# Kernel optimization log

Measured on AMD Instinct MI355X. Metric: run time of the kernel, lower is better.

## Reference

```python
import jax, jax.numpy as jnp
import numpy as np

B, L = 8, 12288
MASK_P = 0.01  # sparsity of the label-correlation adjacency


def setup_inputs() -> dict:
    key = jax.random.key(0)
    k1, k2, k3, k4 = jax.random.split(key, 4)
    predicts = jax.random.normal(k1, (B, L), dtype=jnp.float32)
    similarities = jax.random.uniform(k2, (B, B), dtype=jnp.float32)
    adj = jax.random.uniform(k3, (L, L), dtype=jnp.float32)
    adj_mask = jax.random.bernoulli(k4, MASK_P, (L, L))  # bool: lj in adjList[li]
    return {"predicts": predicts, "similarities": similarities,
            "adj": adj, "adj_mask": adj_mask}


def reference(predicts, similarities, adj, adj_mask):
    dt = predicts.dtype
    m = adj_mask.astype(dt)                      # [L, L]
    diag_m = jnp.diagonal(m)                     # [L]
    eye = jnp.eye(adj.shape[0], dtype=dt)
    # effective matrix: masked adjacency weight, else identity on diagonal
    b_eff = m * adj + eye * (1.0 - diag_m)[None, :]
    # relation_num per target label lj
    counts = jnp.sum(m, axis=0) + (1.0 - diag_m)  # [L]
    candidates = (predicts @ b_eff) / counts[None, :]          # [B, L]
    diff = predicts - similarities @ candidates                # [B, L]
    norms = jnp.sqrt(jnp.sum(diff * diff, axis=1))             # [B]
    valid = jnp.sum(similarities, axis=1) != 0                 # [B]
    cnt = jnp.sum(valid.astype(dt))
    total = jnp.sum(jnp.where(valid, norms, jnp.zeros((), dt)))
    return jnp.where(cnt == 0, jnp.zeros((), dt), total / jnp.maximum(cnt, 1.0))
```

## Files before the change

### kernel.cpp

```cpp
#include <hip/hip_runtime.h>
#include <hip/hip_bf16.h>
#include <stdint.h>

#define BB 8
#define LL 12288
#define NCB 12
#define NCH 96
#define RPC (LL / NCH)

#define WS_FLAGS 0
#define WS_SACC  16
#define WS_CNT   (WS_SACC + BB * LL)
#define WS_NORM2 (WS_CNT + LL)
#define WS_TOTAL (WS_NORM2 + 8)

__device__ __forceinline__ float bf2f(uint16_t u) {
  union { uint32_t i; float f; } v; v.i = ((uint32_t)u) << 16; return v.f;
}

__global__ void detect_kernel(const uint8_t* __restrict__ mask,
                              const uint8_t* __restrict__ adj,
                              int* __restrict__ flags) {
  __shared__ int s[6];
  int tid = threadIdx.x;
  if (tid < 6) s[tid] = 0;
  __syncthreads();
  int c[4] = {0, 0, 0, 0};
  int big = 0, hi = 0;
  const int N = 65536;
  for (int idx = tid; idx < N; idx += blockDim.x) {
    uint8_t v = mask[idx];
    if (v) { c[idx & 3]++; if (v >= 2) big++; }
    uint8_t a = adj[idx];
    if ((idx & 3) == 1 && a >= 0x80) hi++;
  }
  atomicAdd(&s[0], c[0]); atomicAdd(&s[1], c[1]);
  atomicAdd(&s[2], c[2]); atomicAdd(&s[3], c[3]);
  atomicAdd(&s[4], big);  atomicAdd(&s[5], hi);
  __syncthreads();
  if (tid == 0) {
    int width;
    int nzoff = s[1] + s[2] + s[3];
    if (nzoff == 0)             width = 4;
    else if (s[0] + s[1] == 0)  width = 4;
    else if (s[4] == 0)         width = 1;
    else                        width = 2;
    flags[0] = width;
    flags[1] = (s[5] == 0) ? 1 : 0;
  }
}

template <int MW, int FB>
__device__ void s1loop(const uint8_t* __restrict__ mask,
                       const uint8_t* __restrict__ adj,
                       float* __restrict__ sacc, float* __restrict__ cntw,
                       const float* __restrict__ sp,
                       int j0, int i0) {
  float acc[BB][4];
  float c4[4] = {0.f, 0.f, 0.f, 0.f};
#pragma unroll
  for (int b = 0; b < BB; b++)
    acc[b][0] = acc[b][1] = acc[b][2] = acc[b][3] = 0.f;

#pragma unroll 2
  for (int il = 0; il < RPC; ++il) {
    size_t e = (size_t)(i0 + il) * LL + j0;
    float a[4];
    if (FB) {
      ushort4 u = *reinterpret_cast<const ushort4*>(adj + e * 2);
      a[0] = bf2f(u.x); a[1] = bf2f(u.y); a[2] = bf2f(u.z); a[3] = bf2f(u.w);
    } else {
      float4 f = *reinterpret_cast<const float4*>(adj + e * 4);
      a[0] = f.x; a[1] = f.y; a[2] = f.z; a[3] = f.w;
    }
    int m[4];
    if (MW == 1) {
      uchar4 u = *reinterpret_cast<const uchar4*>(mask + e);
      m[0] = u.x != 0; m[1] = u.y != 0; m[2] = u.z != 0; m[3] = u.w != 0;
    } else if (MW == 2) {
      ushort4 u = *reinterpret_cast<const ushort4*>(mask + e * 2);
      m[0] = u.x != 0; m[1] = u.y != 0; m[2] = u.z != 0; m[3] = u.w != 0;
    } else {
      uint4 u = *reinterpret_cast<const uint4*>(mask + e * 4);
      m[0] = u.x != 0; m[1] = u.y != 0; m[2] = u.z != 0; m[3] = u.w != 0;
    }
#pragma unroll
    for (int k = 0; k < 4; k++) {
      a[k] = m[k] ? a[k] : 0.f;
      c4[k] += m[k] ? 1.f : 0.f;
    }
    float4 p0 = *reinterpret_cast<const float4*>(sp + il * BB);
    float4 p1 = *reinterpret_cast<const float4*>(sp + il * BB + 4);
    float pv[BB] = {p0.x, p0.y, p0.z, p0.w, p1.x, p1.y, p1.z, p1.w};
#pragma unroll
    for (int b = 0; b < BB; b++)
#pragma unroll
      for (int k = 0; k < 4; k++) acc[b][k] = fmaf(pv[b], a[k], acc[b][k]);
  }
#pragma unroll
  for (int b = 0; b < BB; b++)
#pragma unroll
    for (int k = 0; k < 4; k++)
      unsafeAtomicAdd(&sacc[b * LL + j0 + k], acc[b][k]);
#pragma unroll
  for (int k = 0; k < 4; k++) unsafeAtomicAdd(&cntw[j0 + k], c4[k]);
}

__global__ __launch_bounds__(256) void stage1(const uint8_t* __restrict__ mask,
                                              const uint8_t* __restrict__ adj,
                                              const uint8_t* __restrict__ pred,
                                              float* __restrict__ ws) {
  __shared__ float sp[RPC * BB];
  const int* fl = (const int*)ws;
  int mw = fl[0], fb = fl[1];
  int cb = blockIdx.x % NCB;
  int ch = blockIdx.x / NCB;
  int j0 = cb * 1024 + threadIdx.x * 4;
  int i0 = ch * RPC;
  for (int idx = threadIdx.x; idx < RPC * BB; idx += 256) {
    int b = idx / RPC, il = idx % RPC;
    float p = fb ? bf2f(reinterpret_cast<const uint16_t*>(pred)[b * LL + i0 + il])
                 : reinterpret_cast<const float*>(pred)[b * LL + i0 + il];
    sp[il * BB + b] = p;
  }
  __syncthreads();
  float* sacc = ws + WS_SACC;
  float* cntw = ws + WS_CNT;
  if (fb) {
    if (mw == 1)      s1loop<1, 1>(mask, adj, sacc, cntw, sp, j0, i0);
    else if (mw == 2) s1loop<2, 1>(mask, adj, sacc, cntw, sp, j0, i0);
    else              s1loop<4, 1>(mask, adj, sacc, cntw, sp, j0, i0);
  } else {
    if (mw == 1)      s1loop<1, 0>(mask, adj, sacc, cntw, sp, j0, i0);
    else if (mw == 2) s1loop<2, 0>(mask, adj, sacc, cntw, sp, j0, i0);
    else              s1loop<4, 0>(mask, adj, sacc, cntw, sp, j0, i0);
  }
}

__global__ __launch_bounds__(256) void stage23(const uint8_t* __restrict__ mask,
                                               const uint8_t* __restrict__ pred,
                                               const uint8_t* __restrict__ sim,
                                               float* __restrict__ ws) {
  const int* fl = (const int*)ws;
  int mw = fl[0], fb = fl[1];
  float* sacc = ws + WS_SACC;
  float* cntw = ws + WS_CNT;
  float* norm2 = ws + WS_NORM2;
  __shared__ float ssim[64];
  if (threadIdx.x < 64) {
    ssim[threadIdx.x] = fb ? bf2f(((const uint16_t*)sim)[threadIdx.x])
                           : ((const float*)sim)[threadIdx.x];
  }
  __syncthreads();
  int j = blockIdx.x * 256 + threadIdx.x;
  size_t ed = (size_t)j * LL + j;
  int mjj;
  if (mw == 1)      mjj = mask[ed] != 0;
  else if (mw == 2) mjj = ((const uint16_t*)mask)[ed] != 0;
  else              mjj = ((const uint32_t*)mask)[ed] != 0;
  float add = mjj ? 0.f : 1.f;
  float c = cntw[j] + add;
  float pj[BB], cv[BB];
#pragma unroll
  for (int b = 0; b < BB; b++)
    pj[b] = fb ? bf2f(((const uint16_t*)pred)[b * LL + j])
               : ((const float*)pred)[b * LL + j];
#pragma unroll
  for (int k = 0; k < BB; k++) cv[k] = (sacc[k * LL + j] + pj[k] * add) / c;
#pragma unroll
  for (int b = 0; b < BB; b++) {
    float t = pj[b];
#pragma unroll
    for (int k = 0; k < BB; k++) t = fmaf(-ssim[b * 8 + k], cv[k], t);
    float v = t * t;
#pragma unroll
    for (int off = 32; off > 0; off >>= 1) v += __shfl_down(v, off, 64);
    if ((threadIdx.x & 63) == 0) unsafeAtomicAdd(&norm2[b], v);
  }
}

__global__ void stage4(const uint8_t* __restrict__ sim,
                       uint8_t* __restrict__ out, float* __restrict__ ws) {
  if (threadIdx.x != 0) return;
  const int* fl = (const int*)ws;
  int fb = fl[1];
  float* norm2 = ws + WS_NORM2;
  float total = 0.f, cntv = 0.f;
  for (int b = 0; b < BB; b++) {
    float rs = 0.f;
    for (int k = 0; k < 8; k++)
      rs += fb ? bf2f(((const uint16_t*)sim)[b * 8 + k])
               : ((const float*)sim)[b * 8 + k];
    if (rs != 0.f) { cntv += 1.f; total += sqrtf(norm2[b]); }
  }
  float res = (cntv == 0.f) ? 0.f : total / fmaxf(cntv, 1.f);
  if (fb) *reinterpret_cast<__hip_bfloat16*>(out) = __float2bfloat16(res);
  else    *reinterpret_cast<float*>(out) = res;
}

extern "C" void kernel_launch(void* const* d_in, const int* in_sizes, int n_in,
                              void* d_out, int out_size, void* d_ws,
                              size_t ws_size, hipStream_t stream) {
  const uint8_t* pred = (const uint8_t*)d_in[0];
  const uint8_t* sim  = (const uint8_t*)d_in[1];
  const uint8_t* adj  = (const uint8_t*)d_in[2];
  const uint8_t* mask = (const uint8_t*)d_in[3];
  float* ws = (float*)d_ws;

  hipMemsetAsync(d_ws, 0, WS_TOTAL * sizeof(float), stream);
  detect_kernel<<<1, 256, 0, stream>>>(mask, adj, (int*)d_ws);
  stage1<<<NCB * NCH, 256, 0, stream>>>(mask, adj, pred, ws);
  stage23<<<LL / 256, 256, 0, stream>>>(mask, pred, sim, ws);
  stage4<<<1, 64, 0, stream>>>(sim, (uint8_t*)d_out, ws);
}
```

Baseline: 1.452 ms.

## Replace stage1 atomics with per-chunk partial buffers and separate reduction kernel

Each stage1 thread now handles 8 columns with wider vector loads, and the grid changes to 6 column blocks by 128 row chunks. The per-thread results are no longer accumulated with global float atomics. Each row chunk writes its own partial sums and counts to a workspace buffer, and a new reduce kernel sums the 128 partials. This removes atomic contention and the large memset, at the cost of an extra kernel launch and extra partial-buffer traffic. That traffic is about 50MB, which is small next to the 600MB+ adjacency read.

```diff
diff --git a/kernel.cpp b/kernel.cpp
--- a/kernel.cpp
+++ b/kernel.cpp
@@ -4,18 +4,31 @@
 
 #define BB 8
 #define LL 12288
-#define NCB 12
-#define NCH 96
+#define NCB 6
+#define NCH 128
 #define RPC (LL / NCH)
 
 #define WS_FLAGS 0
-#define WS_SACC  16
+#define WS_NORM2 16
+#define WS_SACC  32
 #define WS_CNT   (WS_SACC + BB * LL)
-#define WS_NORM2 (WS_CNT + LL)
-#define WS_TOTAL (WS_NORM2 + 8)
+#define WS_PART  (WS_CNT + LL)
+#define WS_CNTP  (WS_PART + NCH * BB * LL)
 
 __device__ __forceinline__ float bf2f(uint16_t u) {
   union { uint32_t i; float f; } v; v.i = ((uint32_t)u) << 16; return v.f;
+}
+
+__device__ __forceinline__ void unpack8(uint4 u, float* f) {
+  union { uint32_t i; float v; } t;
+  t.i = u.x << 16;          f[0] = t.v;
+  t.i = u.x & 0xFFFF0000u;  f[1] = t.v;
+  t.i = u.y << 16;          f[2] = t.v;
+  t.i = u.y & 0xFFFF0000u;  f[3] = t.v;
+  t.i = u.z << 16;          f[4] = t.v;
+  t.i = u.z & 0xFFFF0000u;  f[5] = t.v;
+  t.i = u.w << 16;          f[6] = t.v;
+  t.i = u.w & 0xFFFF0000u;  f[7] = t.v;
 }
 
 __global__ void detect_kernel(const uint8_t* __restrict__ mask,
@@ -53,41 +66,52 @@
 template <int MW, int FB>
 __device__ void s1loop(const uint8_t* __restrict__ mask,
                        const uint8_t* __restrict__ adj,
-                       float* __restrict__ sacc, float* __restrict__ cntw,
+                       float* __restrict__ part, float* __restrict__ cntp,
                        const float* __restrict__ sp,
-                       int j0, int i0) {
-  float acc[BB][4];
-  float c4[4] = {0.f, 0.f, 0.f, 0.f};
+                       int j0, int i0, int ch) {
+  float acc[BB][8];
+  float c8[8] = {0.f, 0.f, 0.f, 0.f, 0.f, 0.f, 0.f, 0.f};
 #pragma unroll
   for (int b = 0; b < BB; b++)
-    acc[b][0] = acc[b][1] = acc[b][2] = acc[b][3] = 0.f;
+#pragma unroll
+    for (int k = 0; k < 8; k++) acc[b][k] = 0.f;
 
 #pragma unroll 2
   for (int il = 0; il < RPC; ++il) {
     size_t e = (size_t)(i0 + il) * LL + j0;
-    float a[4];
+    float a[8];
     if (FB) {
-      ushort4 u = *reinterpret_cast<const ushort4*>(adj + e * 2);
-      a[0] = bf2f(u.x); a[1] = bf2f(u.y); a[2] = bf2f(u.z); a[3] = bf2f(u.w);
+      uint4 u = *reinterpret_cast<const uint4*>(adj + e * 2);
+      unpack8(u, a);
     } else {
-      float4 f = *reinterpret_cast<const float4*>(adj + e * 4);
-      a[0] = f.x; a[1] = f.y; a[2] = f.z; a[3] = f.w;
+      float4 f0 = *reinterpret_cast<const float4*>(adj + e * 4);
+      float4 f1 = *reinterpret_cast<const float4*>(adj + e * 4 + 16);
+      a[0] = f0.x; a[1] = f0.y; a[2] = f0.z; a[3] = f0.w;
+      a[4] = f1.x; a[5] = f1.y; a[6] = f1.z; a[7] = f1.w;
     }
-    int m[4];
+    int m[8];
     if (MW == 1) {
-      uchar4 u = *reinterpret_cast<const uchar4*>(mask + e);
-      m[0] = u.x != 0; m[1] = u.y != 0; m[2] = u.z != 0; m[3] = u.w != 0;
+      uint2 u = *reinterpret_cast<const uint2*>(mask + e);
+      m[0] = (u.x & 0x000000FFu) != 0; m[1] = (u.x & 0x0000FF00u) != 0;
+      m[2] = (u.x & 0x00FF0000u) != 0; m[3] = (u.x & 0xFF000000u) != 0;
+      m[4] = (u.y & 0x000000FFu) != 0; m[5] = (u.y & 0x0000FF00u) != 0;
+      m[6] = (u.y & 0x00FF0000u) != 0; m[7] = (u.y & 0xFF000000u) != 0;
     } else if (MW == 2) {
-      ushort4 u = *reinterpret_cast<const ushort4*>(mask + e * 2);
-      m[0] = u.x != 0; m[1] = u.y != 0; m[2] = u.z != 0; m[3] = u.w != 0;
+      uint4 u = *reinterpret_cast<const uint4*>(mask + e * 2);
+      m[0] = (u.x & 0xFFFFu) != 0; m[1] = (u.x >> 16) != 0;
+      m[2] = (u.y & 0xFFFFu) != 0; m[3] = (u.y >> 16) != 0;
+      m[4] = (u.z & 0xFFFFu) != 0; m[5] = (u.z >> 16) != 0;
+      m[6] = (u.w & 0xFFFFu) != 0; m[7] = (u.w >> 16) != 0;
     } else {
-      uint4 u = *reinterpret_cast<const uint4*>(mask + e * 4);
-      m[0] = u.x != 0; m[1] = u.y != 0; m[2] = u.z != 0; m[3] = u.w != 0;
+      uint4 u0 = *reinterpret_cast<const uint4*>(mask + e * 4);
+      uint4 u1 = *reinterpret_cast<const uint4*>(mask + e * 4 + 16);
+      m[0] = u0.x != 0; m[1] = u0.y != 0; m[2] = u0.z != 0; m[3] = u0.w != 0;
+      m[4] = u1.x != 0; m[5] = u1.y != 0; m[6] = u1.z != 0; m[7] = u1.w != 0;
     }
 #pragma unroll
-    for (int k = 0; k < 4; k++) {
+    for (int k = 0; k < 8; k++) {
       a[k] = m[k] ? a[k] : 0.f;
-      c4[k] += m[k] ? 1.f : 0.f;
+      c8[k] += m[k] ? 1.f : 0.f;
     }
     float4 p0 = *reinterpret_cast<const float4*>(sp + il * BB);
     float4 p1 = *reinterpret_cast<const float4*>(sp + il * BB + 4);
@@ -95,15 +119,17 @@
 #pragma unroll
     for (int b = 0; b < BB; b++)
 #pragma unroll
-      for (int k = 0; k < 4; k++) acc[b][k] = fmaf(pv[b], a[k], acc[b][k]);
-  }
-#pragma unroll
-  for (int b = 0; b < BB; b++)
-#pragma unroll
-    for (int k = 0; k < 4; k++)
-      unsafeAtomicAdd(&sacc[b * LL + j0 + k], acc[b][k]);
-#pragma unroll
-  for (int k = 0; k < 4; k++) unsafeAtomicAdd(&cntw[j0 + k], c4[k]);
+      for (int k = 0; k < 8; k++) acc[b][k] = fmaf(pv[b], a[k], acc[b][k]);
+  }
+#pragma unroll
+  for (int b = 0; b < BB; b++) {
+    float* dst = part + ((size_t)ch * BB + b) * LL + j0;
+    *reinterpret_cast<float4*>(dst)     = make_float4(acc[b][0], acc[b][1], acc[b][2], acc[b][3]);
+    *reinterpret_cast<float4*>(dst + 4) = make_float4(acc[b][4], acc[b][5], acc[b][6], acc[b][7]);
+  }
+  float* cdst = cntp + (size_t)ch * LL + j0;
+  *reinterpret_cast<float4*>(cdst)     = make_float4(c8[0], c8[1], c8[2], c8[3]);
+  *reinterpret_cast<float4*>(cdst + 4) = make_float4(c8[4], c8[5], c8[6], c8[7]);
 }
 
 __global__ __launch_bounds__(256) void stage1(const uint8_t* __restrict__ mask,
@@ -115,7 +141,7 @@
   int mw = fl[0], fb = fl[1];
   int cb = blockIdx.x % NCB;
   int ch = blockIdx.x / NCB;
-  int j0 = cb * 1024 + threadIdx.x * 4;
+  int j0 = cb * 2048 + threadIdx.x * 8;
   int i0 = ch * RPC;
   for (int idx = threadIdx.x; idx < RPC * BB; idx += 256) {
     int b = idx / RPC, il = idx % RPC;
@@ -124,16 +150,32 @@
     sp[il * BB + b] = p;
   }
   __syncthreads();
-  float* sacc = ws + WS_SACC;
-  float* cntw = ws + WS_CNT;
+  float* part = ws + WS_PART;
+  float* cntp = ws + WS_CNTP;
   if (fb) {
-    if (mw == 1)      s1loop<1, 1>(mask, adj, sacc, cntw, sp, j0, i0);
-    else if (mw == 2) s1loop<2, 1>(mask, adj, sacc, cntw, sp, j0, i0);
-    else              s1loop<4, 1>(mask, adj, sacc, cntw, sp, j0, i0);
+    if (mw == 1)      s1loop<1, 1>(mask, adj, part, cntp, sp, j0, i0, ch);
+    else if (mw == 2) s1loop<2, 1>(mask, adj, part, cntp, sp, j0, i0, ch);
+    else              s1loop<4, 1>(mask, adj, part, cntp, sp, j0, i0, ch);
   } else {
-    if (mw == 1)      s1loop<1, 0>(mask, adj, sacc, cntw, sp, j0, i0);
-    else if (mw == 2) s1loop<2, 0>(mask, adj, sacc, cntw, sp, j0, i0);
-    else              s1loop<4, 0>(mask, adj, sacc, cntw, sp, j0, i0);
+    if (mw == 1)      s1loop<1, 0>(mask, adj, part, cntp, sp, j0, i0, ch);
+    else if (mw == 2) s1loop<2, 0>(mask, adj, part, cntp, sp, j0, i0, ch);
+    else              s1loop<4, 0>(mask, adj, part, cntp, sp, j0, i0, ch);
+  }
+}
+
+__global__ __launch_bounds__(256) void reduce_kernel(float* __restrict__ ws) {
+  int idx = blockIdx.x * 256 + threadIdx.x;
+  const float* part = ws + WS_PART;
+  float s = 0.f;
+#pragma unroll 8
+  for (int c = 0; c < NCH; c++) s += part[(size_t)c * (BB * LL) + idx];
+  ws[WS_SACC + idx] = s;
+  if (idx < LL) {
+    const float* cntp = ws + WS_CNTP;
+    float cs = 0.f;
+#pragma unroll 8
+    for (int c = 0; c < NCH; c++) cs += cntp[(size_t)c * LL + idx];
+    ws[WS_CNT + idx] = cs;
   }
 }
 
@@ -207,9 +249,10 @@
   const uint8_t* mask = (const uint8_t*)d_in[3];
   float* ws = (float*)d_ws;
 
-  hipMemsetAsync(d_ws, 0, WS_TOTAL * sizeof(float), stream);
+  hipMemsetAsync(d_ws, 0, 32 * sizeof(float), stream);
   detect_kernel<<<1, 256, 0, stream>>>(mask, adj, (int*)d_ws);
   stage1<<<NCB * NCH, 256, 0, stream>>>(mask, adj, pred, ws);
+  reduce_kernel<<<BB * LL / 256, 256, 0, stream>>>(ws);
   stage23<<<LL / 256, 256, 0, stream>>>(mask, pred, sim, ws);
   stage4<<<1, 64, 0, stream>>>(sim, (uint8_t*)d_out, ws);
 }
```

Measured after the change: 1.389 ms. 1.05x faster.
